# Optimization experiments

Hardware: AMD Instinct MI355X
Metric: run time of the kernel (lower is better)

## Reference

```python
import jax, jax.numpy as jnp
import numpy as np

B, N, L, C, H = 2, 300, 16384, 256, 8
DH = C // H
HID = 4 * C
SCALE = DH ** -0.5
EPS = 1e-5


def layernorm(x, g, b):
    m = x.mean(-1, keepdims=True)
    v = ((x - m) ** 2).mean(-1, keepdims=True)
    return (x - m) * jax.lax.rsqrt(v + EPS) * g + b


def setup_inputs() -> dict:
    key = jax.random.key(0)
    ks = jax.random.split(key, 12)
    w = lambda k, shape: jax.random.normal(k, shape, jnp.float32) * 0.02
    return {
        "query": jax.random.normal(ks[0], (B, N, C), jnp.float32),
        "key": jax.random.normal(ks[1], (B, L, C), jnp.float32),
        "value": jax.random.normal(ks[2], (B, L, C), jnp.float32),
        "key_padding_mask": jnp.zeros((B, L), bool),  # no padding
        "Wq": w(ks[3], (C, C)),
        "Wk": w(ks[4], (C, C)),
        "Wv": w(ks[5], (C, C)),
        "Wp": w(ks[6], (C, C)), "bp": jnp.zeros((C,), jnp.float32),
        "Wg1": w(ks[7], (H, H)), "bg1": jnp.zeros((H,), jnp.float32),
        "Wg2": w(ks[8], (H, 1)), "bg2": jnp.zeros((1,), jnp.float32),
        "ln1_g": jnp.ones((C,), jnp.float32), "ln1_b": jnp.zeros((C,), jnp.float32),
        "W1": w(ks[9], (C, HID)), "b1": jnp.zeros((HID,), jnp.float32),
        "W2": w(ks[10], (HID, C)), "b2": jnp.zeros((C,), jnp.float32),
        "ln2_g": jnp.ones((C,), jnp.float32), "ln2_b": jnp.zeros((C,), jnp.float32),
    }


def reference(query, key, value, key_padding_mask, Wq, Wk, Wv, Wp, bp,
              Wg1, bg1, Wg2, bg2, ln1_g, ln1_b, W1, b1, W2, b2, ln2_g, ln2_b):
    # ---- attention with score-gated mask MLP ----
    q = (query @ Wq).reshape(B, N, H, DH).transpose(0, 2, 1, 3)  # b h n d
    k = (key @ Wk).reshape(B, L, H, DH).transpose(0, 2, 1, 3)    # b h l d
    v = (value @ Wv).reshape(B, L, H, DH).transpose(0, 2, 1, 3)  # b h l d
    attn = jnp.einsum('bhnd,bhld->bhnl', q, k) * SCALE           # raw scores
    attn = jnp.where(key_padding_mask[:, None, None, :], -jnp.inf, attn)
    # gate MLP on RAW scores, per (b,n,l) position over heads: H->H->1, sigmoid
    s = attn.transpose(0, 2, 3, 1)                               # b n l h
    mask = jax.nn.sigmoid(jax.nn.relu(s @ Wg1 + bg1) @ Wg2 + bg2)  # b n l 1
    a = jax.nn.softmax(attn, axis=-1)
    x = jnp.einsum('bhnl,bhld->bnhd', a, v).reshape(B, N, C)
    x = x @ Wp + bp
    # ---- post-norm residual + MLP ----
    out = layernorm(query + x, ln1_g, ln1_b)
    ffn = jax.nn.gelu(out @ W1 + b1, approximate=False) @ W2 + b2
    out = layernorm(out + ffn, ln2_g, ln2_b)
    return (out, mask)
```

## Files before the change

kernel.cpp:

```cpp
#include <hip/hip_runtime.h>
#include <hip/hip_bf16.h>
#include <math.h>

typedef __attribute__((ext_vector_type(4))) float f32x4;
typedef __attribute__((ext_vector_type(8))) short short8;

#define DEV static __device__ __forceinline__

static constexpr int T_B = 2, T_N = 300, T_L = 16384, T_C = 256;
static constexpr int NCH = 64;
static constexpr float ATT_SCALE = 0.17677669529663687f;

DEV unsigned short f2bf(float f) {
  unsigned u = __builtin_bit_cast(unsigned, f);
  u += 0x7FFFu + ((u >> 16) & 1u);
  return (unsigned short)(u >> 16);
}

DEV f32x4 mfma_bf16(short8 a, short8 b, f32x4 c) {
  return __builtin_amdgcn_mfma_f32_16x16x32_bf16(a, b, c, 0, 0, 0);
}

__global__ __launch_bounds__(256) void prep_k(
    const float* __restrict__ Wq, const float* __restrict__ Wk,
    const float* __restrict__ Wv, const float* __restrict__ Wp,
    const float* __restrict__ W1, const float* __restrict__ W2,
    unsigned short* __restrict__ out)
{
  const int idx = blockIdx.x * 256 + threadIdx.x;
  if (idx < 262144) {
    const int w = idx >> 16, rel = idx & 65535;
    const float* src = (w == 0) ? Wq : (w == 1) ? Wk : (w == 2) ? Wv : Wp;
    const int n = rel >> 8, k = rel & 255;
    out[(w << 16) + rel] = f2bf(src[(size_t)k * 256 + n]);
  } else if (idx < 524288) {
    const int rel = idx - 262144;
    const int n = rel >> 8, k = rel & 255;
    out[262144 + rel] = f2bf(W1[(size_t)k * 1024 + n]);
  } else {
    const int rel = idx - 524288;
    const int n = rel >> 10, k = rel & 1023;
    out[524288 + rel] = f2bf(W2[(size_t)k * 256 + n]);
  }
}

template<int BM, int BN, bool ABF, int EPI, bool SPLITK>
__global__ __launch_bounds__(256) void gemm_k(
    const void* __restrict__ Ap, const unsigned short* __restrict__ Bt,
    int M, int N, int K, int ksl,
    void* __restrict__ outp, const float* __restrict__ bias,
    const float* __restrict__ resid)
{
  constexpr int MT = (BM == 128) ? 4 : 1;
  constexpr int NT = (BN == 128) ? ((BM == 128) ? 4 : 8) : 4;
  __shared__ short As[BM][40];
  __shared__ short Bs[BN][40];

  const int tid = threadIdx.x;
  const int w = tid >> 6, j = tid & 63, jr = j & 15, jg = j >> 4;
  const int nct = N / BN;
  const int rt = blockIdx.x / nct, ctb = blockIdx.x - rt * nct;
  const int row0 = rt * BM, n0 = ctb * BN;
  int wrow, wcol;
  if constexpr (BM == 128) { wrow = (w >> 1) << 6; wcol = (w & 1) << 6; }
  else                     { wrow = w << 4;        wcol = 0; }
  const int z = SPLITK ? blockIdx.y : 0;
  const int kbeg = z * ksl;

  f32x4 acc[MT][NT];
#pragma unroll
  for (int a = 0; a < MT; ++a)
#pragma unroll
    for (int b = 0; b < NT; ++b) { acc[a][b][0]=0.f; acc[a][b][1]=0.f; acc[a][b][2]=0.f; acc[a][b][3]=0.f; }

  for (int kk = 0; kk < ksl; kk += 32) {
    const int k0 = kbeg + kk;
    __syncthreads();
    if constexpr (BM == 128) {
      const int r = tid >> 1, ks = (tid & 1) << 4;
      const int gr = row0 + r;
      short tmp[16];
      if (gr < M) {
        if constexpr (ABF) {
          const unsigned short* A = (const unsigned short*)Ap + (size_t)gr * K + k0 + ks;
          *(short8*)&tmp[0] = *(const short8*)A;
          *(short8*)&tmp[8] = *(const short8*)(A + 8);
        } else {
          const float* A = (const float*)Ap + (size_t)gr * K + k0 + ks;
#pragma unroll
          for (int i = 0; i < 4; ++i) {
            float4 v = ((const float4*)A)[i];
            tmp[i*4+0] = (short)f2bf(v.x); tmp[i*4+1] = (short)f2bf(v.y);
            tmp[i*4+2] = (short)f2bf(v.z); tmp[i*4+3] = (short)f2bf(v.w);
          }
        }
      } else {
#pragma unroll
        for (int i = 0; i < 16; ++i) tmp[i] = 0;
      }
      *(short8*)&As[r][ks]   = *(short8*)&tmp[0];
      *(short8*)&As[r][ks+8] = *(short8*)&tmp[8];
    } else {
      const int r = tid >> 2, ks = (tid & 3) << 3;
      const int gr = row0 + r;
      short tmp[8];
      if (gr < M) {
        if constexpr (ABF) {
          *(short8*)tmp = *(const short8*)((const unsigned short*)Ap + (size_t)gr * K + k0 + ks);
        } else {
          const float* A = (const float*)Ap + (size_t)gr * K + k0 + ks;
#pragma unroll
          for (int i = 0; i < 2; ++i) {
            float4 v = ((const float4*)A)[i];
            tmp[i*4+0] = (short)f2bf(v.x); tmp[i*4+1] = (short)f2bf(v.y);
            tmp[i*4+2] = (short)f2bf(v.z); tmp[i*4+3] = (short)f2bf(v.w);
          }
        }
      } else {
#pragma unroll
        for (int i = 0; i < 8; ++i) tmp[i] = 0;
      }
      *(short8*)&As[r][ks] = *(short8*)tmp;
    }
    if constexpr (BN == 128) {
      const int n = tid >> 1, ks = (tid & 1) << 4;
      const unsigned short* bp_ = Bt + (size_t)(n0 + n) * K + k0 + ks;
      *(short8*)&Bs[n][ks]   = *(const short8*)bp_;
      *(short8*)&Bs[n][ks+8] = *(const short8*)(bp_ + 8);
    } else {
      const int n = tid >> 2, ks = (tid & 3) << 3;
      *(short8*)&Bs[n][ks] = *(const short8*)(Bt + (size_t)(n0 + n) * K + k0 + ks);
    }
    __syncthreads();
    short8 af[MT], bfr[NT];
#pragma unroll
    for (int mt = 0; mt < MT; ++mt) af[mt] = *(short8*)&As[wrow + mt*16 + jr][jg*8];
#pragma unroll
    for (int nt = 0; nt < NT; ++nt) bfr[nt] = *(short8*)&Bs[wcol + nt*16 + jr][jg*8];
#pragma unroll
    for (int mt = 0; mt < MT; ++mt)
#pragma unroll
      for (int nt = 0; nt < NT; ++nt)
        acc[mt][nt] = mfma_bf16(af[mt], bfr[nt], acc[mt][nt]);
  }

#pragma unroll
  for (int mt = 0; mt < MT; ++mt)
#pragma unroll
    for (int nt = 0; nt < NT; ++nt)
#pragma unroll
      for (int r = 0; r < 4; ++r) {
        const int m = row0 + wrow + mt*16 + jg*4 + r;
        const int n = n0 + wcol + nt*16 + jr;
        if (m < M) {
          const float v = acc[mt][nt][r];
          if constexpr (EPI == 0) {
            ((unsigned short*)outp)[(size_t)m * N + n] = f2bf(v);
          } else if constexpr (EPI == 1) {
            ((float*)outp)[(size_t)m * N + n] = v + bias[n] + resid[(size_t)m * N + n];
          } else if constexpr (EPI == 2) {
            const float x = v + bias[n];
            ((unsigned short*)outp)[(size_t)m * N + n] =
                f2bf(0.5f * x * (1.f + erff(x * 0.70710678118654752f)));
          } else {
            float* o = (float*)outp + (size_t)z * M * N;
            o[(size_t)m * N + n] = v + ((z == 0) ? bias[n] : 0.f);
          }
        }
      }
}

__global__ __launch_bounds__(256) void gemmT_k(
    const unsigned short* __restrict__ WvT, const float* __restrict__ value,
    unsigned short* __restrict__ vpT)
{
  __shared__ short As[128][40];
  __shared__ short Bs[128][40];
  const int tid = threadIdx.x;
  const int w = tid >> 6, j = tid & 63, jr = j & 15, jg = j >> 4;
  const int b = blockIdx.y;
  const int rt = blockIdx.x >> 7, ctb = blockIdx.x & 127;
  const int row0 = rt << 7, n0 = ctb << 7;
  const int wrow = (w >> 1) << 6, wcol = (w & 1) << 6;

  f32x4 acc[4][4];
#pragma unroll
  for (int a = 0; a < 4; ++a)
#pragma unroll
    for (int c = 0; c < 4; ++c) { acc[a][c][0]=0.f; acc[a][c][1]=0.f; acc[a][c][2]=0.f; acc[a][c][3]=0.f; }

  for (int k0 = 0; k0 < 256; k0 += 32) {
    __syncthreads();
    {
      const int r = tid >> 1, ks = (tid & 1) << 4;
      const unsigned short* A = WvT + (size_t)(row0 + r) * 256 + k0 + ks;
      *(short8*)&As[r][ks]   = *(const short8*)A;
      *(short8*)&As[r][ks+8] = *(const short8*)(A + 8);
    }
    {
      const int r = tid >> 1, ks = (tid & 1) << 4;
      const float* B = value + (size_t)(b * T_L + n0 + r) * T_C + k0 + ks;
      short tmp[16];
#pragma unroll
      for (int i = 0; i < 4; ++i) {
        float4 v = ((const float4*)B)[i];
        tmp[i*4+0] = (short)f2bf(v.x); tmp[i*4+1] = (short)f2bf(v.y);
        tmp[i*4+2] = (short)f2bf(v.z); tmp[i*4+3] = (short)f2bf(v.w);
      }
      *(short8*)&Bs[r][ks]   = *(short8*)&tmp[0];
      *(short8*)&Bs[r][ks+8] = *(short8*)&tmp[8];
    }
    __syncthreads();
    short8 af[4], bfr[4];
#pragma unroll
    for (int mt = 0; mt < 4; ++mt) af[mt] = *(short8*)&As[wrow + mt*16 + jr][jg*8];
#pragma unroll
    for (int nt = 0; nt < 4; ++nt) bfr[nt] = *(short8*)&Bs[wcol + nt*16 + jr][jg*8];
#pragma unroll
    for (int mt = 0; mt < 4; ++mt)
#pragma unroll
      for (int nt = 0; nt < 4; ++nt)
        acc[mt][nt] = mfma_bf16(af[mt], bfr[nt], acc[mt][nt]);
  }
#pragma unroll
  for (int mt = 0; mt < 4; ++mt)
#pragma unroll
    for (int nt = 0; nt < 4; ++nt)
#pragma unroll
      for (int r = 0; r < 4; ++r) {
        const int m = row0 + wrow + mt*16 + jg*4 + r;
        const int n = n0 + wcol + nt*16 + jr;
        vpT[(size_t)(b * T_C + m) * T_L + n] = f2bf(acc[mt][nt][r]);
      }
}

__global__ __launch_bounds__(256, 4) void gate_k(
    const unsigned short* __restrict__ qp, const unsigned short* __restrict__ kp,
    const float* __restrict__ Wg1, const float* __restrict__ bg1,
    const float* __restrict__ Wg2, const float* __restrict__ bg2,
    float* __restrict__ maskout)
{
  __shared__ unsigned short Ks[32][264];
  const int tid = threadIdx.x, w = tid >> 6, j = tid & 63;
  const int jr = j & 15, jg = j >> 4;
  const int bid = blockIdx.x;
  const int chg = bid & 127;
  const int nt5 = (bid >> 7) % 5;
  const int b = bid / 640;
  const int n0w = nt5 * 64 + w * 16;

  short8 qf[8];
  {
    const int nq = n0w + jr;
    const bool ok = nq < T_N;
    const unsigned short* qbase = qp + (size_t)(b * T_N + (ok ? nq : 0)) * T_C + jg * 8;
    short8 zz = {0,0,0,0,0,0,0,0};
#pragma unroll
    for (int h = 0; h < 8; ++h) {
      short8 v = *(const short8*)(qbase + h * 32);
      qf[h] = ok ? v : zz;
    }
  }
  const float vbg2 = bg2[0];

  for (int st = 0; st < 4; ++st) {
    const int l0 = chg * 128 + st * 32;
    __syncthreads();
    {
      const int row = tid >> 3, cb = (tid & 7) << 5;
      const unsigned short* src = kp + (size_t)(b * T_L + l0 + row) * T_C + cb;
      *(short8*)&Ks[row][cb]      = *(const short8*)src;
      *(short8*)&Ks[row][cb + 8]  = *(const short8*)(src + 8);
      *(short8*)&Ks[row][cb + 16] = *(const short8*)(src + 16);
      *(short8*)&Ks[row][cb + 24] = *(const short8*)(src + 24);
    }
    __syncthreads();
#pragma unroll
    for (int ct = 0; ct < 2; ++ct) {
      float tac[4][8];
#pragma unroll
      for (int r = 0; r < 4; ++r)
#pragma unroll
        for (int q = 0; q < 8; ++q) tac[r][q] = bg1[q];
#pragma unroll
      for (int h = 0; h < 8; ++h) {
        const short8 kf = *(const short8*)&Ks[ct*16 + jr][h*32 + jg*8];
        f32x4 fz = {0.f, 0.f, 0.f, 0.f};
        const f32x4 s = mfma_bf16(qf[h], kf, fz);
#pragma unroll
        for (int r = 0; r < 4; ++r) {
          const float a = s[r] * ATT_SCALE;
#pragma unroll
          for (int q = 0; q < 8; ++q)
            tac[r][q] = __builtin_fmaf(a, Wg1[h*8 + q], tac[r][q]);
        }
      }
#pragma unroll
      for (int r = 0; r < 4; ++r) {
        float acc = vbg2;
#pragma unroll
        for (int q = 0; q < 8; ++q)
          acc = __builtin_fmaf(fmaxf(tac[r][q], 0.f), Wg2[q], acc);
        const float g = 1.f / (1.f + __expf(-acc));
        const int ng = n0w + jg*4 + r;
        if (ng < T_N)
          __builtin_nontemporal_store(g,
              &maskout[(size_t)(b * T_N + ng) * T_L + l0 + ct*16 + jr]);
      }
    }
  }
}

__global__ __launch_bounds__(256, 4) void pv_k(
    const unsigned short* __restrict__ qp, const unsigned short* __restrict__ kp,
    const unsigned short* __restrict__ vpT,
    float* __restrict__ Opart, float* __restrict__ Spart)
{
  __shared__ unsigned short Ks[32][136];
  __shared__ unsigned short Vs[128][40];
  __shared__ unsigned short Ps[4][16][40];
  const int tid = threadIdx.x, w = tid >> 6, j = tid & 63;
  const int jr = j & 15, jg = j >> 4;
  const int bid = blockIdx.x;
  const int hg = bid & 1;
  const int ch = (bid >> 1) & 63;
  const int nt5 = (bid >> 7) % 5;
  const int b = bid / 640;
  const int n0w = nt5 * 64 + w * 16;

  short8 qf[4];
  {
    const int nq = n0w + jr;
    const bool ok = nq < T_N;
    const unsigned short* qbase = qp + (size_t)(b * T_N + (ok ? nq : 0)) * T_C + hg*128 + jg*8;
    short8 zz = {0,0,0,0,0,0,0,0};
#pragma unroll
    for (int h = 0; h < 4; ++h) {
      short8 v = *(const short8*)(qbase + h * 32);
      qf[h] = ok ? v : zz;
    }
  }

  f32x4 o[4][2], ps[4];
#pragma unroll
  for (int h = 0; h < 4; ++h)
#pragma unroll
    for (int i = 0; i < 4; ++i) { o[h][0][i]=0.f; o[h][1][i]=0.f; ps[h][i]=0.f; }

  for (int st = 0; st < 8; ++st) {
    const int l0 = ch * 256 + st * 32;
    __syncthreads();
    {
      const int row = tid >> 3, cs = (tid & 7) << 4;
      const unsigned short* src = kp + (size_t)(b * T_L + l0 + row) * T_C + hg*128 + cs;
      *(short8*)&Ks[row][cs]     = *(const short8*)src;
      *(short8*)&Ks[row][cs + 8] = *(const short8*)(src + 8);
    }
    {
      const int d = tid >> 1, ls = (tid & 1) << 4;
      const unsigned short* src = vpT + (size_t)(b * T_C + hg*128 + d) * T_L + l0 + ls;
      *(short8*)&Vs[d][ls]     = *(const short8*)src;
      *(short8*)&Vs[d][ls + 8] = *(const short8*)(src + 8);
    }
    __syncthreads();
#pragma unroll
    for (int h = 0; h < 4; ++h) {
      const short8 kf0 = *(const short8*)&Ks[jr][h*32 + jg*8];
      const short8 kf1 = *(const short8*)&Ks[16 + jr][h*32 + jg*8];
      f32x4 fz = {0.f, 0.f, 0.f, 0.f};
      const f32x4 s0 = mfma_bf16(qf[h], kf0, fz);
      const f32x4 s1 = mfma_bf16(qf[h], kf1, fz);
#pragma unroll
      for (int r = 0; r < 4; ++r) {
        const float p0 = __expf(s0[r] * ATT_SCALE);
        const float p1 = __expf(s1[r] * ATT_SCALE);
        ps[h][r] += p0 + p1;
        Ps[w][jg*4 + r][jr]      = f2bf(p0);
        Ps[w][jg*4 + r][16 + jr] = f2bf(p1);
      }
      const short8 pf = *(const short8*)&Ps[w][jr][jg*8];
      o[h][0] = mfma_bf16(pf, *(const short8*)&Vs[h*32 + jr][jg*8],      o[h][0]);
      o[h][1] = mfma_bf16(pf, *(const short8*)&Vs[h*32 + 16 + jr][jg*8], o[h][1]);
    }
  }

#pragma unroll
  for (int h = 0; h < 4; ++h)
#pragma unroll
    for (int r = 0; r < 4; ++r) {
      float v = ps[h][r];
      v += __shfl_xor(v, 1); v += __shfl_xor(v, 2);
      v += __shfl_xor(v, 4); v += __shfl_xor(v, 8);
      ps[h][r] = v;
    }

#pragma unroll
  for (int h = 0; h < 4; ++h)
#pragma unroll
    for (int r = 0; r < 4; ++r) {
      const int ng = n0w + jg*4 + r;
      if (ng < T_N) {
        const size_t rowi = (size_t)ch * 600 + b * T_N + ng;
        if (jr == 0) Spart[rowi * 8 + hg*4 + h] = ps[h][r];
        Opart[rowi * 256 + (hg*4 + h)*32 + jr]      = o[h][0][r];
        Opart[rowi * 256 + (hg*4 + h)*32 + 16 + jr] = o[h][1][r];
      }
    }
}

__global__ __launch_bounds__(256) void combine_k(
    const float* __restrict__ Opart, const float* __restrict__ Spart,
    unsigned short* __restrict__ Xbf)
{
  __shared__ float Ssh[8];
  const int row = blockIdx.x, t = threadIdx.x;
  float X = 0.f;
  const float* op = Opart + (size_t)row * 256 + t;
#pragma unroll 8
  for (int c = 0; c < 64; ++c) X += op[(size_t)c * 153600];
  if (t < 64) {
    const float* sp = Spart + ((size_t)t * 600 + row) * 8;
    float4 a = *(const float4*)sp, bq = *(const float4*)(sp + 4);
#pragma unroll
    for (int m = 1; m < 64; m <<= 1) {
      a.x += __shfl_xor(a.x, m); a.y += __shfl_xor(a.y, m);
      a.z += __shfl_xor(a.z, m); a.w += __shfl_xor(a.w, m);
      bq.x += __shfl_xor(bq.x, m); bq.y += __shfl_xor(bq.y, m);
      bq.z += __shfl_xor(bq.z, m); bq.w += __shfl_xor(bq.w, m);
    }
    if (t == 0) {
      Ssh[0]=a.x; Ssh[1]=a.y; Ssh[2]=a.z; Ssh[3]=a.w;
      Ssh[4]=bq.x; Ssh[5]=bq.y; Ssh[6]=bq.z; Ssh[7]=bq.w;
    }
  }
  __syncthreads();
  Xbf[(size_t)row * 256 + t] = f2bf(X / Ssh[t >> 5]);
}

__global__ __launch_bounds__(256) void ln_k(
    const float* __restrict__ xa, const float* __restrict__ parts, int np,
    const float* __restrict__ gg, const float* __restrict__ bb,
    float* __restrict__ outf, unsigned short* __restrict__ outbf)
{
  __shared__ float sA[4], sB[4];
  const int row = blockIdx.x, c = threadIdx.x, w = c >> 6;
  const size_t i = (size_t)row * T_C + c;
  float v = xa[i];
  for (int p = 0; p < np; ++p) v += parts[(size_t)p * 153600 + i];
  float s = v;
  for (int m = 1; m < 64; m <<= 1) s += __shfl_xor(s, m);
  if ((c & 63) == 0) sA[w] = s;
  __syncthreads();
  const float mean = (sA[0]+sA[1]+sA[2]+sA[3]) * (1.f/256.f);
  const float dv = v - mean;
  float q = dv*dv;
  for (int m = 1; m < 64; m <<= 1) q += __shfl_xor(q, m);
  if ((c & 63) == 0) sB[w] = q;
  __syncthreads();
  const float var = (sB[0]+sB[1]+sB[2]+sB[3]) * (1.f/256.f);
  const float y = dv * rsqrtf(var + 1e-5f) * gg[c] + bb[c];
  if (outf)  outf[i] = y;
  if (outbf) outbf[i] = f2bf(y);
}

extern "C" void kernel_launch(void* const* d_in, const int* in_sizes, int n_in,
                              void* d_out, int out_size, void* d_ws, size_t ws_size,
                              hipStream_t stream) {
  const float* query = (const float*)d_in[0];
  const float* key   = (const float*)d_in[1];
  const float* value = (const float*)d_in[2];
  const float* Wq  = (const float*)d_in[4];
  const float* Wk  = (const float*)d_in[5];
  const float* Wv  = (const float*)d_in[6];
  const float* Wp  = (const float*)d_in[7];
  const float* bp  = (const float*)d_in[8];
  const float* Wg1 = (const float*)d_in[9];
  const float* bg1 = (const float*)d_in[10];
  const float* Wg2 = (const float*)d_in[11];
  const float* bg2 = (const float*)d_in[12];
  const float* ln1g = (const float*)d_in[13];
  const float* ln1b = (const float*)d_in[14];
  const float* W1  = (const float*)d_in[15];
  const float* b1  = (const float*)d_in[16];
  const float* W2  = (const float*)d_in[17];
  const float* b2  = (const float*)d_in[18];
  const float* ln2g = (const float*)d_in[19];
  const float* ln2b = (const float*)d_in[20];

  char* ws = (char*)d_ws;
  unsigned short* WqT  = (unsigned short*)(ws + 0);
  unsigned short* WkT  = (unsigned short*)(ws + 131072);
  unsigned short* WvT  = (unsigned short*)(ws + 262144);
  unsigned short* WpT  = (unsigned short*)(ws + 393216);
  unsigned short* W1T  = (unsigned short*)(ws + 524288);
  unsigned short* W2T  = (unsigned short*)(ws + 1048576);
  unsigned short* qp   = (unsigned short*)(ws + 1572864);
  unsigned short* kp   = (unsigned short*)(ws + 1880064);
  unsigned short* vpT  = (unsigned short*)(ws + 18657280);
  float*          Opart= (float*)(ws + 35434496);
  float*          Spart= (float*)(ws + 74756096);
  unsigned short* Xbf  = (unsigned short*)(ws + 75984896);
  float*          t1   = (float*)(ws + 76292096);
  float*          ln1f = (float*)(ws + 76906496);
  unsigned short* ln1bf= (unsigned short*)(ws + 77520896);
  unsigned short* hbf  = (unsigned short*)(ws + 77828096);
  float*          t2p  = (float*)(ws + 79056896);

  float* outMain = (float*)d_out;
  float* outMask = outMain + 153600;

  hipLaunchKernelGGL(prep_k, dim3(3072), dim3(256), 0, stream,
                     Wq, Wk, Wv, Wp, W1, W2, (unsigned short*)ws);

  hipLaunchKernelGGL((gemm_k<64,64,false,0,false>), dim3(40), dim3(256), 0, stream,
                     (const void*)query, WqT, 600, 256, 256, 256, (void*)qp, nullptr, nullptr);
  hipLaunchKernelGGL((gemm_k<128,128,false,0,false>), dim3(512), dim3(256), 0, stream,
                     (const void*)key, WkT, 32768, 256, 256, 256, (void*)kp, nullptr, nullptr);
  hipLaunchKernelGGL(gemmT_k, dim3(256, 2), dim3(256), 0, stream, WvT, value, vpT);

  hipLaunchKernelGGL(gate_k, dim3(1280), dim3(256), 0, stream,
                     qp, kp, Wg1, bg1, Wg2, bg2, outMask);
  hipLaunchKernelGGL(pv_k, dim3(1280), dim3(256), 0, stream,
                     qp, kp, vpT, Opart, Spart);
  hipLaunchKernelGGL(combine_k, dim3(600), dim3(256), 0, stream, Opart, Spart, Xbf);

  hipLaunchKernelGGL((gemm_k<64,64,true,1,false>), dim3(40), dim3(256), 0, stream,
                     (const void*)Xbf, WpT, 600, 256, 256, 256, (void*)t1, bp, query);
  hipLaunchKernelGGL(ln_k, dim3(600), dim3(256), 0, stream,
                     t1, (const float*)nullptr, 0, ln1g, ln1b, ln1f, ln1bf);

  hipLaunchKernelGGL((gemm_k<64,64,true,2,false>), dim3(160), dim3(256), 0, stream,
                     (const void*)ln1bf, W1T, 600, 1024, 256, 256, (void*)hbf, b1, nullptr);
  hipLaunchKernelGGL((gemm_k<64,64,true,3,true>), dim3(40, 4), dim3(256), 0, stream,
                     (const void*)hbf, W2T, 600, 256, 1024, 256, (void*)t2p, b2, nullptr);
  hipLaunchKernelGGL(ln_k, dim3(600), dim3(256), 0, stream,
                     ln1f, t2p, 4, ln2g, ln2b, outMain, (unsigned short*)nullptr);
}
```

Baseline: 298.0 us.

## Merge projection GEMMs and gate/PV attention kernels into combined launches

Folds the Q, K and V projection GEMMs into one launch that dispatches on block index, and interleaves the gate-MLP and PV attention blocks into a single kernel using dynamic shared memory. The intent is to cut launch overhead and tail idle time between dependent-free kernels, and to let the memory-bound gate blocks overlap with the MFMA-bound PV blocks on the same CUs. The PV body also gives each head its own P staging tile so all four heads' exp/stores finish before the PV MFMAs. This costs more shared memory per block, since attn_k reserves the larger footprint for both roles, which may lower occupancy for gate blocks.

New measurement: 288.6 us. 3.2% less time.

```diff
diff --git a/kernel.cpp b/kernel.cpp
--- a/kernel.cpp
+++ b/kernel.cpp
@@ -45,7 +45,7 @@
 }
 
 template<int BM, int BN, bool ABF, int EPI, bool SPLITK>
-__global__ __launch_bounds__(256) void gemm_k(
+DEV void gemm_body(char* smem, int lbid, int z,
     const void* __restrict__ Ap, const unsigned short* __restrict__ Bt,
     int M, int N, int K, int ksl,
     void* __restrict__ outp, const float* __restrict__ bias,
@@ -53,18 +53,17 @@
 {
   constexpr int MT = (BM == 128) ? 4 : 1;
   constexpr int NT = (BN == 128) ? ((BM == 128) ? 4 : 8) : 4;
-  __shared__ short As[BM][40];
-  __shared__ short Bs[BN][40];
+  short (*As)[40] = (short(*)[40])smem;
+  short (*Bs)[40] = (short(*)[40])(smem + BM * 80);
 
   const int tid = threadIdx.x;
   const int w = tid >> 6, j = tid & 63, jr = j & 15, jg = j >> 4;
   const int nct = N / BN;
-  const int rt = blockIdx.x / nct, ctb = blockIdx.x - rt * nct;
+  const int rt = lbid / nct, ctb = lbid - rt * nct;
   const int row0 = rt * BM, n0 = ctb * BN;
   int wrow, wcol;
   if constexpr (BM == 128) { wrow = (w >> 1) << 6; wcol = (w & 1) << 6; }
   else                     { wrow = w << 4;        wcol = 0; }
-  const int z = SPLITK ? blockIdx.y : 0;
   const int kbeg = z * ksl;
 
   f32x4 acc[MT][NT];
@@ -170,16 +169,29 @@
       }
 }
 
-__global__ __launch_bounds__(256) void gemmT_k(
+template<int BM, int BN, bool ABF, int EPI, bool SPLITK>
+__global__ __launch_bounds__(256) void gemm_k(
+    const void* __restrict__ Ap, const unsigned short* __restrict__ Bt,
+    int M, int N, int K, int ksl,
+    void* __restrict__ outp, const float* __restrict__ bias,
+    const float* __restrict__ resid)
+{
+  extern __shared__ char smem[];
+  gemm_body<BM,BN,ABF,EPI,SPLITK>(smem, blockIdx.x, SPLITK ? blockIdx.y : 0,
+                                  Ap, Bt, M, N, K, ksl, outp, bias, resid);
+}
+
+DEV void gemmT_body(char* smem, int lbid,
     const unsigned short* __restrict__ WvT, const float* __restrict__ value,
     unsigned short* __restrict__ vpT)
 {
-  __shared__ short As[128][40];
-  __shared__ short Bs[128][40];
+  short (*As)[40] = (short(*)[40])smem;
+  short (*Bs)[40] = (short(*)[40])(smem + 128 * 80);
   const int tid = threadIdx.x;
   const int w = tid >> 6, j = tid & 63, jr = j & 15, jg = j >> 4;
-  const int b = blockIdx.y;
-  const int rt = blockIdx.x >> 7, ctb = blockIdx.x & 127;
+  const int b = lbid >> 8;
+  const int idx = lbid & 255;
+  const int rt = idx >> 7, ctb = idx & 127;
   const int row0 = rt << 7, n0 = ctb << 7;
   const int wrow = (w >> 1) << 6, wcol = (w & 1) << 6;
 
@@ -234,19 +246,38 @@
       }
 }
 
-__global__ __launch_bounds__(256, 4) void gate_k(
+__global__ __launch_bounds__(256) void proj_k(
+    const float* __restrict__ query, const unsigned short* __restrict__ WqT,
+    const float* __restrict__ key,   const unsigned short* __restrict__ WkT,
+    const float* __restrict__ value, const unsigned short* __restrict__ WvT,
+    unsigned short* __restrict__ qp, unsigned short* __restrict__ kp,
+    unsigned short* __restrict__ vpT)
+{
+  extern __shared__ char smem[];
+  const int bid = blockIdx.x;
+  if (bid < 512) {
+    gemm_body<128,128,false,0,false>(smem, bid, 0, (const void*)key, WkT,
+                                     32768, 256, 256, 256, (void*)kp, nullptr, nullptr);
+  } else if (bid < 1024) {
+    gemmT_body(smem, bid - 512, WvT, value, vpT);
+  } else {
+    gemm_body<64,64,false,0,false>(smem, bid - 1024, 0, (const void*)query, WqT,
+                                   600, 256, 256, 256, (void*)qp, nullptr, nullptr);
+  }
+}
+
+DEV void gate_body(char* smem, int gbid,
     const unsigned short* __restrict__ qp, const unsigned short* __restrict__ kp,
     const float* __restrict__ Wg1, const float* __restrict__ bg1,
     const float* __restrict__ Wg2, const float* __restrict__ bg2,
     float* __restrict__ maskout)
 {
-  __shared__ unsigned short Ks[32][264];
+  unsigned short (*Ks)[264] = (unsigned short(*)[264])smem;
   const int tid = threadIdx.x, w = tid >> 6, j = tid & 63;
   const int jr = j & 15, jg = j >> 4;
-  const int bid = blockIdx.x;
-  const int chg = bid & 127;
-  const int nt5 = (bid >> 7) % 5;
-  const int b = bid / 640;
+  const int chg = gbid & 127;
+  const int nt5 = (gbid >> 7) % 5;
+  const int b = gbid / 640;
   const int n0w = nt5 * 64 + w * 16;
 
   short8 qf[8];
@@ -311,21 +342,20 @@
   }
 }
 
-__global__ __launch_bounds__(256, 4) void pv_k(
+DEV void pv_body(char* smem, int pbid,
     const unsigned short* __restrict__ qp, const unsigned short* __restrict__ kp,
     const unsigned short* __restrict__ vpT,
     float* __restrict__ Opart, float* __restrict__ Spart)
 {
-  __shared__ unsigned short Ks[32][136];
-  __shared__ unsigned short Vs[128][40];
-  __shared__ unsigned short Ps[4][16][40];
+  unsigned short (*Ks)[136]     = (unsigned short(*)[136])smem;
+  unsigned short (*Vs)[40]      = (unsigned short(*)[40])(smem + 8704);
+  unsigned short (*Ps)[16][40]  = (unsigned short(*)[16][40])(smem + 18944);
   const int tid = threadIdx.x, w = tid >> 6, j = tid & 63;
   const int jr = j & 15, jg = j >> 4;
-  const int bid = blockIdx.x;
-  const int hg = bid & 1;
-  const int ch = (bid >> 1) & 63;
-  const int nt5 = (bid >> 7) % 5;
-  const int b = bid / 640;
+  const int hg = pbid & 1;
+  const int ch = (pbid >> 1) & 63;
+  const int nt5 = (pbid >> 7) % 5;
+  const int b = pbid / 640;
   const int n0w = nt5 * 64 + w * 16;
 
   short8 qf[4];
@@ -370,15 +400,19 @@
       f32x4 fz = {0.f, 0.f, 0.f, 0.f};
       const f32x4 s0 = mfma_bf16(qf[h], kf0, fz);
       const f32x4 s1 = mfma_bf16(qf[h], kf1, fz);
+      unsigned short (*Ph)[40] = Ps[(w << 2) | h];
 #pragma unroll
       for (int r = 0; r < 4; ++r) {
         const float p0 = __expf(s0[r] * ATT_SCALE);
         const float p1 = __expf(s1[r] * ATT_SCALE);
         ps[h][r] += p0 + p1;
-        Ps[w][jg*4 + r][jr]      = f2bf(p0);
-        Ps[w][jg*4 + r][16 + jr] = f2bf(p1);
-      }
-      const short8 pf = *(const short8*)&Ps[w][jr][jg*8];
+        Ph[jg*4 + r][jr]      = f2bf(p0);
+        Ph[jg*4 + r][16 + jr] = f2bf(p1);
+      }
+    }
+#pragma unroll
+    for (int h = 0; h < 4; ++h) {
+      const short8 pf = *(const short8*)&Ps[(w << 2) | h][jr][jg*8];
       o[h][0] = mfma_bf16(pf, *(const short8*)&Vs[h*32 + jr][jg*8],      o[h][0]);
       o[h][1] = mfma_bf16(pf, *(const short8*)&Vs[h*32 + 16 + jr][jg*8], o[h][1]);
     }
@@ -406,6 +440,19 @@
         Opart[rowi * 256 + (hg*4 + h)*32 + 16 + jr] = o[h][1][r];
       }
     }
+}
+
+__global__ __launch_bounds__(256, 4) void attn_k(
+    const unsigned short* __restrict__ qp, const unsigned short* __restrict__ kp,
+    const unsigned short* __restrict__ vpT,
+    const float* __restrict__ Wg1, const float* __restrict__ bg1,
+    const float* __restrict__ Wg2, const float* __restrict__ bg2,
+    float* __restrict__ maskout, float* __restrict__ Opart, float* __restrict__ Spart)
+{
+  extern __shared__ char smem[];
+  const int bid = blockIdx.x;
+  if (bid & 1) pv_body(smem, bid >> 1, qp, kp, vpT, Opart, Spart);
+  else         gate_body(smem, bid >> 1, qp, kp, Wg1, bg1, Wg2, bg2, maskout);
 }
 
 __global__ __launch_bounds__(256) void combine_k(
@@ -512,26 +559,22 @@
   hipLaunchKernelGGL(prep_k, dim3(3072), dim3(256), 0, stream,
                      Wq, Wk, Wv, Wp, W1, W2, (unsigned short*)ws);
 
-  hipLaunchKernelGGL((gemm_k<64,64,false,0,false>), dim3(40), dim3(256), 0, stream,
-                     (const void*)query, WqT, 600, 256, 256, 256, (void*)qp, nullptr, nullptr);
-  hipLaunchKernelGGL((gemm_k<128,128,false,0,false>), dim3(512), dim3(256), 0, stream,
-                     (const void*)key, WkT, 32768, 256, 256, 256, (void*)kp, nullptr, nullptr);
-  hipLaunchKernelGGL(gemmT_k, dim3(256, 2), dim3(256), 0, stream, WvT, value, vpT);
-
-  hipLaunchKernelGGL(gate_k, dim3(1280), dim3(256), 0, stream,
-                     qp, kp, Wg1, bg1, Wg2, bg2, outMask);
-  hipLaunchKernelGGL(pv_k, dim3(1280), dim3(256), 0, stream,
-                     qp, kp, vpT, Opart, Spart);
+  hipLaunchKernelGGL(proj_k, dim3(1064), dim3(256), 20480, stream,
+                     query, WqT, key, WkT, value, WvT, qp, kp, vpT);
+
+  hipLaunchKernelGGL(attn_k, dim3(2560), dim3(256), 39424, stream,
+                     qp, kp, vpT, Wg1, bg1, Wg2, bg2, outMask, Opart, Spart);
+
   hipLaunchKernelGGL(combine_k, dim3(600), dim3(256), 0, stream, Opart, Spart, Xbf);
 
-  hipLaunchKernelGGL((gemm_k<64,64,true,1,false>), dim3(40), dim3(256), 0, stream,
+  hipLaunchKernelGGL((gemm_k<64,64,true,1,false>), dim3(40), dim3(256), 10240, stream,
                      (const void*)Xbf, WpT, 600, 256, 256, 256, (void*)t1, bp, query);
   hipLaunchKernelGGL(ln_k, dim3(600), dim3(256), 0, stream,
                      t1, (const float*)nullptr, 0, ln1g, ln1b, ln1f, ln1bf);
 
-  hipLaunchKernelGGL((gemm_k<64,64,true,2,false>), dim3(160), dim3(256), 0, stream,
+  hipLaunchKernelGGL((gemm_k<64,64,true,2,false>), dim3(160), dim3(256), 10240, stream,
                      (const void*)ln1bf, W1T, 600, 1024, 256, 256, (void*)hbf, b1, nullptr);
-  hipLaunchKernelGGL((gemm_k<64,64,true,3,true>), dim3(40, 4), dim3(256), 0, stream,
+  hipLaunchKernelGGL((gemm_k<64,64,true,3,true>), dim3(40, 4), dim3(256), 10240, stream,
                      (const void*)hbf, W2T, 600, 256, 1024, 256, (void*)t2p, b2, nullptr);
   hipLaunchKernelGGL(ln_k, dim3(600), dim3(256), 0, stream,
                      ln1f, t2p, 4, ln2g, ln2b, outMain, (unsigned short*)nullptr);
```
